# Kernel tuning notes

Hardware: AMD Instinct MI355X
Metric: run time of the kernel (lower is better)

The kernel has to match this reference:

```python
import jax, jax.numpy as jnp
import numpy as np


def _pairwise_sqdist(a, b):
    # a: [m, n, d], b: [m, n, d] -> M: [m, n, n], M[m,i,j] = ||a[m,i]-b[m,j]||^2
    # Use the expansion |a|^2 + |b|^2 - 2 a.b to avoid materializing the
    # [m, n, n, d] difference tensor; clamp tiny negatives from cancellation.
    a2 = jnp.sum(a * a, axis=-1)  # [m, n]
    b2 = jnp.sum(b * b, axis=-1)  # [m, n]
    ab = jnp.einsum('mid,mjd->mij', a, b)  # [m, n, n]
    return jnp.maximum(a2[:, :, None] + b2[:, None, :] - 2.0 * ab, 0.0)


def setup_inputs() -> dict:
    key = jax.random.key(0)
    k1, k2 = jax.random.split(key)
    template = jax.random.normal(k1, (16, 4096, 3), dtype=jnp.float32)
    source = jax.random.normal(k2, (16, 4096, 3), dtype=jnp.float32)
    return {"template": template, "source": source}


def reference(template, source):
    M = _pairwise_sqdist(template, source)  # [m, n, n]
    # min over template index (axis 1): nearest template point for each source point
    dist1 = jnp.mean(jnp.sqrt(jnp.min(M, axis=1)))
    # min over source index (axis 2): nearest source point for each template point
    dist2 = jnp.mean(jnp.sqrt(jnp.min(M, axis=2)))
    return (dist1 + dist2) / 2.0
```

## Files before the change

### kernel.cpp

```cpp
#include <hip/hip_runtime.h>

#define N_PTS   4096
#define N_BATCH 16
#define INV_CNT (1.0f / (2.0f * N_BATCH * N_PTS))
#define AROW_BYTES ((size_t)2 * N_BATCH * N_PTS * 16 * 2)
#define NBLK    512

typedef _Float16 f16x8  __attribute__((ext_vector_type(8)));

__global__ __launch_bounds__(256) void prep_kernel(
    const float* __restrict__ tpl, const float* __restrict__ src,
    _Float16* __restrict__ arow, float* __restrict__ out) {
    int pt = blockIdx.x * 256 + threadIdx.x;
    if (pt == 0) out[0] = 0.0f;
    const float* p = (pt < 65536 ? tpl : src) + (size_t)(pt & 65535) * 3;
    float x = p[0], y = p[1], z = p[2];
    float o2 = fmaf(x, x, fmaf(y, y, z * z));
    _Float16 xh = (_Float16)x, yh = (_Float16)y, zh = (_Float16)z;
    _Float16 xl = (_Float16)(x - (float)xh);
    _Float16 yl = (_Float16)(y - (float)yh);
    _Float16 zl = (_Float16)(z - (float)zh);
    _Float16 o2h = (_Float16)o2;
    _Float16 o2l = (_Float16)(o2 - (float)o2h);
    const _Float16 m2 = (_Float16)-2.0f;
    f16x8 v0, v1;
    v0[0] = m2 * xh; v0[1] = m2 * yh; v0[2] = m2 * zh;
    v0[3] = m2 * xl; v0[4] = m2 * yl; v0[5] = m2 * zl;
    v0[6] = m2 * xh; v0[7] = m2 * yh;
    v1[0] = m2 * zh; v1[1] = o2h; v1[2] = o2l;
    v1[3] = (_Float16)0.0f; v1[4] = (_Float16)0.0f; v1[5] = (_Float16)0.0f;
    v1[6] = (_Float16)0.0f; v1[7] = (_Float16)0.0f;
    *(f16x8*)(arow + (size_t)pt * 16)     = v0;
    *(f16x8*)(arow + (size_t)pt * 16 + 8) = v1;
}

#define FD(a,x,y) "v_min3_f32 %[" #a "], v" #x ", v" #y ", %[" #a "]\n\t"
#define FOLD_D0A FD(acc0,32,33) FD(acc1,34,35) FD(acc0,36,37) FD(acc1,38,39) \
                 FD(acc0,40,41) FD(acc1,42,43) FD(acc0,44,45) FD(acc1,46,47)
#define FOLD_D0B FD(acc0,48,49) FD(acc1,50,51) FD(acc0,52,53) FD(acc1,54,55) \
                 FD(acc0,56,57) FD(acc1,58,59) FD(acc0,60,61) FD(acc1,62,63)
#define FOLD_D1A FD(acc2,64,65) FD(acc3,66,67) FD(acc2,68,69) FD(acc3,70,71) \
                 FD(acc2,72,73) FD(acc3,74,75) FD(acc2,76,77) FD(acc3,78,79)
#define FOLD_D1B FD(acc2,80,81) FD(acc3,82,83) FD(acc2,84,85) FD(acc3,86,87) \
                 FD(acc2,88,89) FD(acc3,90,91) FD(acc2,92,93) FD(acc3,94,95)
#define LD(s,off) "global_load_dwordx4 %[" #s "], %[voff], %[sb] offset:" #off "\n\t"
#define TILE_E(s,off) "s_waitcnt vmcnt(7)\n\t" \
  "v_mfma_f32_32x32x16_f16 v[32:47], %[" #s "], %[bf0], v[96:111]\n\t" \
  "v_mfma_f32_32x32x16_f16 v[64:79], %[" #s "], %[bf1], v[96:111]\n\t" \
  LD(s,off) FOLD_D0B FOLD_D1B
#define TILE_O(s,off) "s_waitcnt vmcnt(7)\n\t" \
  "v_mfma_f32_32x32x16_f16 v[48:63], %[" #s "], %[bf0], v[96:111]\n\t" \
  "v_mfma_f32_32x32x16_f16 v[80:95], %[" #s "], %[bf1], v[96:111]\n\t" \
  LD(s,off) FOLD_D0A FOLD_D1A
#define ZM(r)  "v_mov_b32 v" #r ", 0\n\t"
#define IM(r)  "v_mov_b32 v" #r ", 0x7f800000\n\t"

__global__ __launch_bounds__(256, 2) void chamfer_mfma(
    const float* __restrict__ tpl, const float* __restrict__ src,
    const _Float16* __restrict__ arow, float* __restrict__ blocksum,
    float* __restrict__ out) {
    __shared__ float wsum[4];

    const int tid = threadIdx.x;
    const int wv = tid >> 6, lane = tid & 63;
    const int n = lane & 31, g = lane >> 5;
    const int lin = blockIdx.x + 16 * (blockIdx.y + 16 * blockIdx.z);
    const int xcd = lin & 7;
    const int s_  = lin >> 3;
    const int qb  = s_ & 15;
    const int region = xcd + 8 * (s_ >> 4);
    const int batch  = region & 15;
    const int dir    = region >> 4;

    const float* qpts = (dir == 0) ? src : tpl;
    const _Float16* abase = arow + ((dir == 0) ? (size_t)0 : (size_t)65536 * 16)
                          + (size_t)batch * 4096 * 16;

    f16x8 bfr[2];
    float p2[2];
    #pragma unroll
    for (int i = 0; i < 2; ++i) {
        const int q = qb * 256 + wv * 64 + i * 32 + n;
        const float* p = qpts + (size_t)(batch * 4096 + q) * 3;
        float px = p[0], py = p[1], pz = p[2];
        p2[i] = fmaf(px, px, fmaf(py, py, pz * pz));
        _Float16 xh = (_Float16)px, yh = (_Float16)py, zh = (_Float16)pz;
        _Float16 xl = (_Float16)(px - (float)xh);
        _Float16 yl = (_Float16)(py - (float)yh);
        _Float16 zl = (_Float16)(pz - (float)zh);
        f16x8 b;
        if (g == 0) {
            b[0] = xh; b[1] = yh; b[2] = zh;
            b[3] = xh; b[4] = yh; b[5] = zh;
            b[6] = xl; b[7] = yl;
        } else {
            b[0] = zl; b[1] = (_Float16)1.0f; b[2] = (_Float16)1.0f;
            b[3] = (_Float16)0.0f; b[4] = (_Float16)0.0f; b[5] = (_Float16)0.0f;
            b[6] = (_Float16)0.0f; b[7] = (_Float16)0.0f;
        }
        bfr[i] = b;
    }

    int voff = n * 32 + g * 16;
    int cnt = 16;
    float acc0 = 1e30f, acc1 = 1e30f, acc2 = 1e30f, acc3 = 1e30f;
    f16x8 r0, r1, r2, r3, r4, r5, r6, r7;

    asm volatile(
        ZM(96) ZM(97) ZM(98) ZM(99) ZM(100) ZM(101) ZM(102) ZM(103)
        ZM(104) ZM(105) ZM(106) ZM(107) ZM(108) ZM(109) ZM(110) ZM(111)
        IM(48) IM(49) IM(50) IM(51) IM(52) IM(53) IM(54) IM(55)
        IM(56) IM(57) IM(58) IM(59) IM(60) IM(61) IM(62) IM(63)
        IM(80) IM(81) IM(82) IM(83) IM(84) IM(85) IM(86) IM(87)
        IM(88) IM(89) IM(90) IM(91) IM(92) IM(93) IM(94) IM(95)
        LD(r0,0) LD(r1,1024) LD(r2,2048) LD(r3,3072)
        "v_add_u32 %[voff], 0x1000, %[voff]\n\t"
        LD(r4,0) LD(r5,1024) LD(r6,2048) LD(r7,3072)
        "v_add_u32 %[voff], 0x1000, %[voff]\n\t"
        "L_cham_%=:\n\t"
        TILE_E(r0,0) TILE_O(r1,1024) TILE_E(r2,2048) TILE_O(r3,3072)
        "v_add_u32 %[voff], 0x1000, %[voff]\n\t"
        TILE_E(r4,0) TILE_O(r5,1024) TILE_E(r6,2048) TILE_O(r7,3072)
        "v_add_u32 %[voff], 0x1000, %[voff]\n\t"
        "s_sub_u32 %[cnt], %[cnt], 1\n\t"
        "s_cmp_lg_u32 %[cnt], 0\n\t"
        "s_cbranch_scc1 L_cham_%=\n\t"
        "s_nop 7\n\t" "s_nop 7\n\t" "s_nop 7\n\t"
        FOLD_D0B FOLD_D1B
        "s_waitcnt vmcnt(0)\n\t"
        : [r0]"=&v"(r0), [r1]"=&v"(r1), [r2]"=&v"(r2), [r3]"=&v"(r3),
          [r4]"=&v"(r4), [r5]"=&v"(r5), [r6]"=&v"(r6), [r7]"=&v"(r7),
          [voff]"+v"(voff), [cnt]"+s"(cnt),
          [acc0]"+v"(acc0), [acc1]"+v"(acc1), [acc2]"+v"(acc2), [acc3]"+v"(acc3)
        : [bf0]"v"(bfr[0]), [bf1]"v"(bfr[1]), [sb]"s"(abase)
        : "memory", "scc",
          "v32","v33","v34","v35","v36","v37","v38","v39",
          "v40","v41","v42","v43","v44","v45","v46","v47",
          "v48","v49","v50","v51","v52","v53","v54","v55",
          "v56","v57","v58","v59","v60","v61","v62","v63",
          "v64","v65","v66","v67","v68","v69","v70","v71",
          "v72","v73","v74","v75","v76","v77","v78","v79",
          "v80","v81","v82","v83","v84","v85","v86","v87",
          "v88","v89","v90","v91","v92","v93","v94","v95",
          "v96","v97","v98","v99","v100","v101","v102","v103",
          "v104","v105","v106","v107","v108","v109","v110","v111");

    float v0 = fminf(acc0, acc1);
    v0 = fminf(v0, __shfl_xor(v0, 32));
    float v1 = fminf(acc2, acc3);
    v1 = fminf(v1, __shfl_xor(v1, 32));
    float d0 = fmaxf(v0 + p2[0], 0.0f);
    float d1 = fmaxf(v1 + p2[1], 0.0f);
    float s = (sqrtf(d0) + sqrtf(d1)) * INV_CNT;
    if (g != 0) s = 0.0f;
    #pragma unroll
    for (int off = 32; off > 0; off >>= 1) s += __shfl_down(s, off);
    if (lane == 0) wsum[wv] = s;
    __syncthreads();
    if (tid == 0) {
        float t = wsum[0] + wsum[1] + wsum[2] + wsum[3];
        if (blocksum) {
            int flat = (dir * N_BATCH + batch) * 16 + qb;
            blocksum[flat] = t;
        } else {
            atomicAdd(out, t);
        }
    }
}

__global__ __launch_bounds__(256) void final_kernel(
    const float* __restrict__ blocksum, float* __restrict__ out) {
    __shared__ float wsum[4];
    float s = 0.0f;
    #pragma unroll
    for (int j = 0; j < NBLK / 256; ++j)
        s += blocksum[j * 256 + threadIdx.x];
    #pragma unroll
    for (int off = 32; off > 0; off >>= 1) s += __shfl_down(s, off);
    if ((threadIdx.x & 63) == 0) wsum[threadIdx.x >> 6] = s;
    __syncthreads();
    if (threadIdx.x == 0) out[0] = wsum[0] + wsum[1] + wsum[2] + wsum[3];
}

extern "C" void kernel_launch(void* const* d_in, const int* in_sizes, int n_in,
                              void* d_out, int out_size, void* d_ws, size_t ws_size,
                              hipStream_t stream) {
    const float* tpl = (const float*)d_in[0];
    const float* src = (const float*)d_in[1];
    float* out = (float*)d_out;
    _Float16* arow = (_Float16*)d_ws;
    const bool roomy = ws_size >= AROW_BYTES + 8192 + NBLK * sizeof(float);
    float* blocksum = roomy ? (float*)((char*)d_ws + AROW_BYTES + 8192) : nullptr;

    hipLaunchKernelGGL(prep_kernel, dim3((2 * N_BATCH * N_PTS) / 256),
                       dim3(256), 0, stream, tpl, src, arow, out);
    dim3 grid(N_PTS / 256, N_BATCH, 2);
    hipLaunchKernelGGL(chamfer_mfma, grid, dim3(256), 0, stream,
                       tpl, src, arow, blocksum, out);
    if (roomy)
        hipLaunchKernelGGL(final_kernel, dim3(1), dim3(256), 0, stream,
                           blocksum, out);
}
```

Before: 75.44 us.

## Stage arow tiles through LDS with async global-to-LDS double buffering

Replaces per-wave direct global loads of the precomputed A rows with block-cooperative global_load_lds into a double-buffered shared-memory tile, then feeds the MFMAs from ds_read_b128. Each block loads every 16 KB chunk once and shares it across its four waves, instead of each wave fetching the whole 128 KB row set itself. This cuts global/L2 traffic by about four. The cost is two barriers per chunk, 32 KB of LDS per block, and a per-chunk pipeline drain with accumulator re-zeroing. The workspace padding offset for blocksum is also removed.

Result: no change. 74.91 us (-0.7%).

```diff
diff --git a/kernel.cpp b/kernel.cpp
--- a/kernel.cpp
+++ b/kernel.cpp
@@ -7,6 +7,8 @@
 #define NBLK    512
 
 typedef _Float16 f16x8  __attribute__((ext_vector_type(8)));
+#define AS1 __attribute__((address_space(1)))
+#define AS3 __attribute__((address_space(3)))
 
 __global__ __launch_bounds__(256) void prep_kernel(
     const float* __restrict__ tpl, const float* __restrict__ src,
@@ -35,40 +37,39 @@
 }
 
 #define FD(a,x,y) "v_min3_f32 %[" #a "], v" #x ", v" #y ", %[" #a "]\n\t"
-#define FOLD_D0A FD(acc0,32,33) FD(acc1,34,35) FD(acc0,36,37) FD(acc1,38,39) \
-                 FD(acc0,40,41) FD(acc1,42,43) FD(acc0,44,45) FD(acc1,46,47)
-#define FOLD_D0B FD(acc0,48,49) FD(acc1,50,51) FD(acc0,52,53) FD(acc1,54,55) \
-                 FD(acc0,56,57) FD(acc1,58,59) FD(acc0,60,61) FD(acc1,62,63)
-#define FOLD_D1A FD(acc2,64,65) FD(acc3,66,67) FD(acc2,68,69) FD(acc3,70,71) \
-                 FD(acc2,72,73) FD(acc3,74,75) FD(acc2,76,77) FD(acc3,78,79)
-#define FOLD_D1B FD(acc2,80,81) FD(acc3,82,83) FD(acc2,84,85) FD(acc3,86,87) \
-                 FD(acc2,88,89) FD(acc3,90,91) FD(acc2,92,93) FD(acc3,94,95)
-#define LD(s,off) "global_load_dwordx4 %[" #s "], %[voff], %[sb] offset:" #off "\n\t"
-#define TILE_E(s,off) "s_waitcnt vmcnt(7)\n\t" \
-  "v_mfma_f32_32x32x16_f16 v[32:47], %[" #s "], %[bf0], v[96:111]\n\t" \
-  "v_mfma_f32_32x32x16_f16 v[64:79], %[" #s "], %[bf1], v[96:111]\n\t" \
-  LD(s,off) FOLD_D0B FOLD_D1B
-#define TILE_O(s,off) "s_waitcnt vmcnt(7)\n\t" \
-  "v_mfma_f32_32x32x16_f16 v[48:63], %[" #s "], %[bf0], v[96:111]\n\t" \
-  "v_mfma_f32_32x32x16_f16 v[80:95], %[" #s "], %[bf1], v[96:111]\n\t" \
-  LD(s,off) FOLD_D0A FOLD_D1A
-#define ZM(r)  "v_mov_b32 v" #r ", 0\n\t"
-#define IM(r)  "v_mov_b32 v" #r ", 0x7f800000\n\t"
+#define FOLD_A FD(acc0,32,33) FD(acc1,34,35) FD(acc0,36,37) FD(acc1,38,39) \
+               FD(acc0,40,41) FD(acc1,42,43) FD(acc0,44,45) FD(acc1,46,47) \
+               FD(acc2,64,65) FD(acc3,66,67) FD(acc2,68,69) FD(acc3,70,71) \
+               FD(acc2,72,73) FD(acc3,74,75) FD(acc2,76,77) FD(acc3,78,79)
+#define FOLD_B FD(acc0,48,49) FD(acc1,50,51) FD(acc0,52,53) FD(acc1,54,55) \
+               FD(acc0,56,57) FD(acc1,58,59) FD(acc0,60,61) FD(acc1,62,63) \
+               FD(acc2,80,81) FD(acc3,82,83) FD(acc2,84,85) FD(acc3,86,87) \
+               FD(acc2,88,89) FD(acc3,90,91) FD(acc2,92,93) FD(acc3,94,95)
+#define MF_A(d) \
+  "v_mfma_f32_32x32x16_f16 v[32:47], %[" #d "], %[bf0], v[96:111]\n\t" \
+  "v_mfma_f32_32x32x16_f16 v[64:79], %[" #d "], %[bf1], v[96:111]\n\t"
+#define MF_B(d) \
+  "v_mfma_f32_32x32x16_f16 v[48:63], %[" #d "], %[bf0], v[96:111]\n\t" \
+  "v_mfma_f32_32x32x16_f16 v[80:95], %[" #d "], %[bf1], v[96:111]\n\t"
+#define DSR(d,off) "ds_read_b128 %[" #d "], %[dsa] offset:" #off "\n\t"
+#define WL(n) "s_waitcnt lgkmcnt(" #n ")\n\t"
+#define ZM(r) "v_mov_b32 v" #r ", 0\n\t"
+#define NOP3 "s_nop 7\n\t" "s_nop 7\n\t" "s_nop 7\n\t"
 
 __global__ __launch_bounds__(256, 2) void chamfer_mfma(
     const float* __restrict__ tpl, const float* __restrict__ src,
     const _Float16* __restrict__ arow, float* __restrict__ blocksum,
     float* __restrict__ out) {
+    __shared__ uint4 sbuf[2][1024];
     __shared__ float wsum[4];
 
     const int tid = threadIdx.x;
     const int wv = tid >> 6, lane = tid & 63;
     const int n = lane & 31, g = lane >> 5;
     const int lin = blockIdx.x + 16 * (blockIdx.y + 16 * blockIdx.z);
-    const int xcd = lin & 7;
     const int s_  = lin >> 3;
     const int qb  = s_ & 15;
-    const int region = xcd + 8 * (s_ >> 4);
+    const int region = (lin & 7) + 8 * (s_ >> 4);
     const int batch  = region & 15;
     const int dir    = region >> 4;
 
@@ -101,57 +102,82 @@
         bfr[i] = b;
     }
 
-    int voff = n * 32 + g * 16;
-    int cnt = 16;
+    const int lane_off = n * 32 + g * 16;
+    const unsigned dsa0 = (unsigned)(size_t)((AS3 char*)&sbuf[0][0]) + lane_off;
+    const unsigned dsa1 = (unsigned)(size_t)((AS3 char*)&sbuf[1][0]) + lane_off;
+
+    const char* gwave = (const char*)abase + wv * 4096 + lane * 16;
+    #define STAGE(ch)                                                          \
+        {                                                                      \
+            const char* gp = gwave + (size_t)(ch) * 16384;                     \
+            AS3 char* lp = (AS3 char*)&sbuf[(ch) & 1][0] + wv * 4096;          \
+            _Pragma("unroll")                                                  \
+            for (int j = 0; j < 4; ++j)                                        \
+                __builtin_amdgcn_global_load_lds(                              \
+                    (const AS1 unsigned*)(gp + j * 1024),                      \
+                    (AS3 unsigned*)(lp + j * 1024), 16, 0, 0);                 \
+        }
+
     float acc0 = 1e30f, acc1 = 1e30f, acc2 = 1e30f, acc3 = 1e30f;
-    f16x8 r0, r1, r2, r3, r4, r5, r6, r7;
-
-    asm volatile(
-        ZM(96) ZM(97) ZM(98) ZM(99) ZM(100) ZM(101) ZM(102) ZM(103)
-        ZM(104) ZM(105) ZM(106) ZM(107) ZM(108) ZM(109) ZM(110) ZM(111)
-        IM(48) IM(49) IM(50) IM(51) IM(52) IM(53) IM(54) IM(55)
-        IM(56) IM(57) IM(58) IM(59) IM(60) IM(61) IM(62) IM(63)
-        IM(80) IM(81) IM(82) IM(83) IM(84) IM(85) IM(86) IM(87)
-        IM(88) IM(89) IM(90) IM(91) IM(92) IM(93) IM(94) IM(95)
-        LD(r0,0) LD(r1,1024) LD(r2,2048) LD(r3,3072)
-        "v_add_u32 %[voff], 0x1000, %[voff]\n\t"
-        LD(r4,0) LD(r5,1024) LD(r6,2048) LD(r7,3072)
-        "v_add_u32 %[voff], 0x1000, %[voff]\n\t"
-        "L_cham_%=:\n\t"
-        TILE_E(r0,0) TILE_O(r1,1024) TILE_E(r2,2048) TILE_O(r3,3072)
-        "v_add_u32 %[voff], 0x1000, %[voff]\n\t"
-        TILE_E(r4,0) TILE_O(r5,1024) TILE_E(r6,2048) TILE_O(r7,3072)
-        "v_add_u32 %[voff], 0x1000, %[voff]\n\t"
-        "s_sub_u32 %[cnt], %[cnt], 1\n\t"
-        "s_cmp_lg_u32 %[cnt], 0\n\t"
-        "s_cbranch_scc1 L_cham_%=\n\t"
-        "s_nop 7\n\t" "s_nop 7\n\t" "s_nop 7\n\t"
-        FOLD_D0B FOLD_D1B
-        "s_waitcnt vmcnt(0)\n\t"
-        : [r0]"=&v"(r0), [r1]"=&v"(r1), [r2]"=&v"(r2), [r3]"=&v"(r3),
-          [r4]"=&v"(r4), [r5]"=&v"(r5), [r6]"=&v"(r6), [r7]"=&v"(r7),
-          [voff]"+v"(voff), [cnt]"+s"(cnt),
-          [acc0]"+v"(acc0), [acc1]"+v"(acc1), [acc2]"+v"(acc2), [acc3]"+v"(acc3)
-        : [bf0]"v"(bfr[0]), [bf1]"v"(bfr[1]), [sb]"s"(abase)
-        : "memory", "scc",
-          "v32","v33","v34","v35","v36","v37","v38","v39",
-          "v40","v41","v42","v43","v44","v45","v46","v47",
-          "v48","v49","v50","v51","v52","v53","v54","v55",
-          "v56","v57","v58","v59","v60","v61","v62","v63",
-          "v64","v65","v66","v67","v68","v69","v70","v71",
-          "v72","v73","v74","v75","v76","v77","v78","v79",
-          "v80","v81","v82","v83","v84","v85","v86","v87",
-          "v88","v89","v90","v91","v92","v93","v94","v95",
-          "v96","v97","v98","v99","v100","v101","v102","v103",
-          "v104","v105","v106","v107","v108","v109","v110","v111");
+    f16x8 d0, d1, d2, d3;
+
+    STAGE(0)
+    #pragma unroll 1
+    for (int c = 0; c < 8; ++c) {
+        if (c < 7) STAGE(c + 1)
+        if (c < 7)
+            asm volatile("s_waitcnt vmcnt(4)\n\ts_barrier" ::: "memory");
+        else
+            asm volatile("s_waitcnt vmcnt(0)\n\ts_barrier" ::: "memory");
+        const unsigned dsa = (c & 1) ? dsa1 : dsa0;
+
+        asm volatile(
+            ZM(96) ZM(97) ZM(98) ZM(99) ZM(100) ZM(101) ZM(102) ZM(103)
+            ZM(104) ZM(105) ZM(106) ZM(107) ZM(108) ZM(109) ZM(110) ZM(111)
+            DSR(d0,0) DSR(d1,1024) DSR(d2,2048) DSR(d3,3072)
+            WL(3) MF_A(d0) DSR(d0,4096) NOP3
+            WL(3) MF_B(d1) DSR(d1,5120)  FOLD_A
+            WL(3) MF_A(d2) DSR(d2,6144)  FOLD_B
+            WL(3) MF_B(d3) DSR(d3,7168)  FOLD_A
+            WL(3) MF_A(d0) DSR(d0,8192)  FOLD_B
+            WL(3) MF_B(d1) DSR(d1,9216)  FOLD_A
+            WL(3) MF_A(d2) DSR(d2,10240) FOLD_B
+            WL(3) MF_B(d3) DSR(d3,11264) FOLD_A
+            WL(3) MF_A(d0) DSR(d0,12288) FOLD_B
+            WL(3) MF_B(d1) DSR(d1,13312) FOLD_A
+            WL(3) MF_A(d2) DSR(d2,14336) FOLD_B
+            WL(3) MF_B(d3) DSR(d3,15360) FOLD_A
+            WL(3) MF_A(d0) FOLD_B
+            WL(2) MF_B(d1) FOLD_A
+            WL(1) MF_A(d2) FOLD_B
+            WL(0) MF_B(d3) FOLD_A
+            NOP3 FOLD_B
+            : [d0]"=&v"(d0), [d1]"=&v"(d1), [d2]"=&v"(d2), [d3]"=&v"(d3),
+              [acc0]"+v"(acc0), [acc1]"+v"(acc1),
+              [acc2]"+v"(acc2), [acc3]"+v"(acc3)
+            : [bf0]"v"(bfr[0]), [bf1]"v"(bfr[1]), [dsa]"v"(dsa)
+            : "memory",
+              "v32","v33","v34","v35","v36","v37","v38","v39",
+              "v40","v41","v42","v43","v44","v45","v46","v47",
+              "v48","v49","v50","v51","v52","v53","v54","v55",
+              "v56","v57","v58","v59","v60","v61","v62","v63",
+              "v64","v65","v66","v67","v68","v69","v70","v71",
+              "v72","v73","v74","v75","v76","v77","v78","v79",
+              "v80","v81","v82","v83","v84","v85","v86","v87",
+              "v88","v89","v90","v91","v92","v93","v94","v95",
+              "v96","v97","v98","v99","v100","v101","v102","v103",
+              "v104","v105","v106","v107","v108","v109","v110","v111");
+
+        asm volatile("s_barrier" ::: "memory");
+    }
 
     float v0 = fminf(acc0, acc1);
     v0 = fminf(v0, __shfl_xor(v0, 32));
     float v1 = fminf(acc2, acc3);
     v1 = fminf(v1, __shfl_xor(v1, 32));
-    float d0 = fmaxf(v0 + p2[0], 0.0f);
-    float d1 = fmaxf(v1 + p2[1], 0.0f);
-    float s = (sqrtf(d0) + sqrtf(d1)) * INV_CNT;
+    float dd0 = fmaxf(v0 + p2[0], 0.0f);
+    float dd1 = fmaxf(v1 + p2[1], 0.0f);
+    float s = (sqrtf(dd0) + sqrtf(dd1)) * INV_CNT;
     if (g != 0) s = 0.0f;
     #pragma unroll
     for (int off = 32; off > 0; off >>= 1) s += __shfl_down(s, off);
@@ -189,8 +215,8 @@
     const float* src = (const float*)d_in[1];
     float* out = (float*)d_out;
     _Float16* arow = (_Float16*)d_ws;
-    const bool roomy = ws_size >= AROW_BYTES + 8192 + NBLK * sizeof(float);
-    float* blocksum = roomy ? (float*)((char*)d_ws + AROW_BYTES + 8192) : nullptr;
+    const bool roomy = ws_size >= AROW_BYTES + NBLK * sizeof(float);
+    float* blocksum = roomy ? (float*)((char*)d_ws + AROW_BYTES) : nullptr;
 
     hipLaunchKernelGGL(prep_kernel, dim3((2 * N_BATCH * N_PTS) / 256),
                        dim3(256), 0, stream, tpl, src, arow, out);
```
